# Kernel tuning notes

Measured on AMD Instinct MI355X. Metric: run time of the kernel, lower is better.

## Reference

```python
import jax, jax.numpy as jnp
import numpy as np

# Dimensions per init_kwargs / input_specs
B, N, C = 8192, 4, 2048          # tokens, expansion_rate, hidden_dim
SINKHORN_ITERS = 20
EPS = 1e-5
ALPHA_INIT = 0.01


def setup_inputs() -> dict:
    key = jax.random.key(0)
    k1, k2 = jax.random.split(key)
    return {
        "x_expanded": jax.random.normal(k1, (B, N, C), dtype=jnp.float32),
        "rmsnorm_weight": jnp.ones((C,), dtype=jnp.float32),   # init: ones
        "H_pre": jnp.zeros((N,), dtype=jnp.float32),            # init: zeros
        "H_post": jnp.zeros((N,), dtype=jnp.float32),           # init: zeros
        "H_res": ALPHA_INIT * jax.random.normal(k2, (N, N), dtype=jnp.float32),
    }


def _sinkhorn(M, iters, eps):
    """Iterative row/column normalization -> (approximately) doubly-stochastic."""
    def body(_, M):
        M = M / (jnp.sum(M, axis=1, keepdims=True) + eps)  # row normalize
        M = M / (jnp.sum(M, axis=0, keepdims=True) + eps)  # col normalize
        return M
    return jax.lax.fori_loop(0, iters, body, M)


def reference(x_expanded, rmsnorm_weight, H_pre, H_post, H_res):
    # RMSNorm over hidden dim C, per (token, branch)
    ms = jnp.mean(x_expanded * x_expanded, axis=-1, keepdims=True)  # [B, N, 1]
    x_norm = x_expanded * jax.lax.rsqrt(ms + EPS) * rmsnorm_weight  # [B, N, C]

    # Manifold-constrained residual mixing matrix (doubly stochastic via Sinkhorn)
    H = _sinkhorn(jnp.exp(H_res), SINKHORN_ITERS, EPS)              # [N, N]

    pre = jax.nn.sigmoid(H_pre)    # [N] input-aggregation weights
    post = jax.nn.sigmoid(H_post)  # [N] output-distribution weights

    # Aggregate normalized branches into a single stream, redistribute,
    # and add the Sinkhorn-mixed residual of the raw branches.
    x_agg = jnp.einsum('n,bnc->bc', pre, x_norm)                     # [B, C]
    y = jnp.einsum('mn,bnc->bmc', H, x_expanded) \
        + post[None, :, None] * x_agg[:, None, :]                    # [B, N, C]
    return y
```

## Files before the change

kernel.cpp:

```cpp
#include <hip/hip_runtime.h>
#include <math.h>

#define B_TOK 8192
#define NB 4
#define CH 2048
#define TPB 512
#define NBLK 1024
#define TOK_PER_BLK 8
#define SINK_ITERS 20
#define EPS 1e-5f

typedef float f32x4 __attribute__((ext_vector_type(4)));

__device__ __forceinline__ float bcast_first(float v) {
    return __uint_as_float(__builtin_amdgcn_readfirstlane(__float_as_uint(v)));
}
__device__ __forceinline__ float read_lane(float v, int l) {
    return __uint_as_float(__builtin_amdgcn_readlane(__float_as_uint(v), l));
}

__global__ __launch_bounds__(TPB) void mhc_fused(
    const float* __restrict__ x,
    const float* __restrict__ w,
    const float* __restrict__ H_pre,
    const float* __restrict__ H_post,
    const float* __restrict__ H_res,
    float* __restrict__ y)
{
    const int t = threadIdx.x;
    const int wave = t >> 6;
    const int lane = t & 63;
    const int b0 = blockIdx.x * TOK_PER_BLK;

    __shared__ f32x4 red4[2][TPB / 64];

    f32x4 xA0, xA1, xA2, xA3, xB0, xB1, xB2, xB3;
    auto xload = [&](int b, f32x4& d0, f32x4& d1, f32x4& d2, f32x4& d3) {
        const f32x4* p = (const f32x4*)x + (size_t)b * (NB * CH / 4) + t;
        d0 = __builtin_nontemporal_load(p);
        d1 = __builtin_nontemporal_load(p + (CH / 4));
        d2 = __builtin_nontemporal_load(p + 2 * (CH / 4));
        d3 = __builtin_nontemporal_load(p + 3 * (CH / 4));
    };
    xload(b0 + 0, xA0, xA1, xA2, xA3);
    xload(b0 + 1, xB0, xB1, xB2, xB3);
    const f32x4 wv = ((const f32x4*)w)[t];

    const int e = lane & 15;
    float v = expf(H_res[e]);
    #pragma unroll 1
    for (int it = 0; it < SINK_ITERS; ++it) {
        float s = v + __shfl_xor(v, 1);
        s += __shfl_xor(s, 2);
        v *= __builtin_amdgcn_rcpf(s + EPS);
        s = v + __shfl_xor(v, 4);
        s += __shfl_xor(s, 8);
        v *= __builtin_amdgcn_rcpf(s + EPS);
    }
    const float H00 = read_lane(v, 0),  H01 = read_lane(v, 1),
                H02 = read_lane(v, 2),  H03 = read_lane(v, 3);
    const float H10 = read_lane(v, 4),  H11 = read_lane(v, 5),
                H12 = read_lane(v, 6),  H13 = read_lane(v, 7);
    const float H20 = read_lane(v, 8),  H21 = read_lane(v, 9),
                H22 = read_lane(v, 10), H23 = read_lane(v, 11);
    const float H30 = read_lane(v, 12), H31 = read_lane(v, 13),
                H32 = read_lane(v, 14), H33 = read_lane(v, 15);

    const float pre0 = bcast_first(1.0f / (1.0f + expf(-H_pre[0])));
    const float pre1 = bcast_first(1.0f / (1.0f + expf(-H_pre[1])));
    const float pre2 = bcast_first(1.0f / (1.0f + expf(-H_pre[2])));
    const float pre3 = bcast_first(1.0f / (1.0f + expf(-H_pre[3])));
    const float ps0  = bcast_first(1.0f / (1.0f + expf(-H_post[0])));
    const float ps1  = bcast_first(1.0f / (1.0f + expf(-H_post[1])));
    const float ps2  = bcast_first(1.0f / (1.0f + expf(-H_post[2])));
    const float ps3  = bcast_first(1.0f / (1.0f + expf(-H_post[3])));

    auto process = [&](int b, f32x4 x0, f32x4 x1, f32x4 x2, f32x4 x3, int ph) {
        float s0 = x0.x * x0.x + x0.y * x0.y + x0.z * x0.z + x0.w * x0.w;
        float s1 = x1.x * x1.x + x1.y * x1.y + x1.z * x1.z + x1.w * x1.w;
        float s2 = x2.x * x2.x + x2.y * x2.y + x2.z * x2.z + x2.w * x2.w;
        float s3 = x3.x * x3.x + x3.y * x3.y + x3.z * x3.z + x3.w * x3.w;
        #pragma unroll
        for (int m = 1; m < 64; m <<= 1) {
            s0 += __shfl_xor(s0, m);
            s1 += __shfl_xor(s1, m);
            s2 += __shfl_xor(s2, m);
            s3 += __shfl_xor(s3, m);
        }
        if (lane == 0) {
            f32x4 pv = { s0, s1, s2, s3 };
            red4[ph][wave] = pv;
        }

        __builtin_amdgcn_sched_barrier(0);
        asm volatile("s_waitcnt lgkmcnt(0)" ::: "memory");
        __builtin_amdgcn_s_barrier();
        __builtin_amdgcn_sched_barrier(0);

        f32x4 r0 = red4[ph][0], r1 = red4[ph][1], r2 = red4[ph][2], r3 = red4[ph][3];
        f32x4 r4 = red4[ph][4], r5 = red4[ph][5], r6 = red4[ph][6], r7 = red4[ph][7];
        float t0 = ((r0.x + r1.x) + (r2.x + r3.x)) + ((r4.x + r5.x) + (r6.x + r7.x));
        float t1 = ((r0.y + r1.y) + (r2.y + r3.y)) + ((r4.y + r5.y) + (r6.y + r7.y));
        float t2 = ((r0.z + r1.z) + (r2.z + r3.z)) + ((r4.z + r5.z) + (r6.z + r7.z));
        float t3 = ((r0.w + r1.w) + (r2.w + r3.w)) + ((r4.w + r5.w) + (r6.w + r7.w));

        const float a0 = pre0 * rsqrtf(t0 * (1.0f / CH) + EPS);
        const float a1 = pre1 * rsqrtf(t1 * (1.0f / CH) + EPS);
        const float a2 = pre2 * rsqrtf(t2 * (1.0f / CH) + EPS);
        const float a3 = pre3 * rsqrtf(t3 * (1.0f / CH) + EPS);

        f32x4 wu;
        wu.x = wv.x * (a0 * x0.x + a1 * x1.x + a2 * x2.x + a3 * x3.x);
        wu.y = wv.y * (a0 * x0.y + a1 * x1.y + a2 * x2.y + a3 * x3.y);
        wu.z = wv.z * (a0 * x0.z + a1 * x1.z + a2 * x2.z + a3 * x3.z);
        wu.w = wv.w * (a0 * x0.w + a1 * x1.w + a2 * x2.w + a3 * x3.w);

        f32x4* yp = (f32x4*)y + (size_t)b * (NB * CH / 4) + t;
        f32x4 o;
        o.x = H00 * x0.x + H01 * x1.x + H02 * x2.x + H03 * x3.x + ps0 * wu.x;
        o.y = H00 * x0.y + H01 * x1.y + H02 * x2.y + H03 * x3.y + ps0 * wu.y;
        o.z = H00 * x0.z + H01 * x1.z + H02 * x2.z + H03 * x3.z + ps0 * wu.z;
        o.w = H00 * x0.w + H01 * x1.w + H02 * x2.w + H03 * x3.w + ps0 * wu.w;
        __builtin_nontemporal_store(o, yp);
        o.x = H10 * x0.x + H11 * x1.x + H12 * x2.x + H13 * x3.x + ps1 * wu.x;
        o.y = H10 * x0.y + H11 * x1.y + H12 * x2.y + H13 * x3.y + ps1 * wu.y;
        o.z = H10 * x0.z + H11 * x1.z + H12 * x2.z + H13 * x3.z + ps1 * wu.z;
        o.w = H10 * x0.w + H11 * x1.w + H12 * x2.w + H13 * x3.w + ps1 * wu.w;
        __builtin_nontemporal_store(o, yp + (CH / 4));
        o.x = H20 * x0.x + H21 * x1.x + H22 * x2.x + H23 * x3.x + ps2 * wu.x;
        o.y = H20 * x0.y + H21 * x1.y + H22 * x2.y + H23 * x3.y + ps2 * wu.y;
        o.z = H20 * x0.z + H21 * x1.z + H22 * x2.z + H23 * x3.z + ps2 * wu.z;
        o.w = H20 * x0.w + H21 * x1.w + H22 * x2.w + H23 * x3.w + ps2 * wu.w;
        __builtin_nontemporal_store(o, yp + 2 * (CH / 4));
        o.x = H30 * x0.x + H31 * x1.x + H32 * x2.x + H33 * x3.x + ps3 * wu.x;
        o.y = H30 * x0.y + H31 * x1.y + H32 * x2.y + H33 * x3.y + ps3 * wu.y;
        o.z = H30 * x0.z + H31 * x1.z + H32 * x2.z + H33 * x3.z + ps3 * wu.z;
        o.w = H30 * x0.w + H31 * x1.w + H32 * x2.w + H33 * x3.w + ps3 * wu.w;
        __builtin_nontemporal_store(o, yp + 3 * (CH / 4));
    };

    process(b0 + 0, xA0, xA1, xA2, xA3, 0);
    xload(b0 + 2, xA0, xA1, xA2, xA3);
    process(b0 + 1, xB0, xB1, xB2, xB3, 1);
    xload(b0 + 3, xB0, xB1, xB2, xB3);
    process(b0 + 2, xA0, xA1, xA2, xA3, 0);
    xload(b0 + 4, xA0, xA1, xA2, xA3);
    process(b0 + 3, xB0, xB1, xB2, xB3, 1);
    xload(b0 + 5, xB0, xB1, xB2, xB3);
    process(b0 + 4, xA0, xA1, xA2, xA3, 0);
    xload(b0 + 6, xA0, xA1, xA2, xA3);
    process(b0 + 5, xB0, xB1, xB2, xB3, 1);
    xload(b0 + 7, xB0, xB1, xB2, xB3);
    process(b0 + 6, xA0, xA1, xA2, xA3, 0);
    process(b0 + 7, xB0, xB1, xB2, xB3, 1);
}

extern "C" void kernel_launch(void* const* d_in, const int* in_sizes, int n_in,
                              void* d_out, int out_size, void* d_ws, size_t ws_size,
                              hipStream_t stream) {
    const float* x      = (const float*)d_in[0];
    const float* wgt    = (const float*)d_in[1];
    const float* h_pre  = (const float*)d_in[2];
    const float* h_post = (const float*)d_in[3];
    const float* h_res  = (const float*)d_in[4];
    float* y = (float*)d_out;

    mhc_fused<<<NBLK, TPB, 0, stream>>>(x, wgt, h_pre, h_post, h_res, y);
}
```

Measured before the change: 102.4 us.

## Assign one token per wave to remove block-level LDS reduction and barriers

```diff
diff --git a/kernel.cpp b/kernel.cpp
--- a/kernel.cpp
+++ b/kernel.cpp
@@ -1,12 +1,11 @@
 #include <hip/hip_runtime.h>
 #include <math.h>
 
-#define B_TOK 8192
 #define NB 4
 #define CH 2048
-#define TPB 512
-#define NBLK 1024
-#define TOK_PER_BLK 8
+#define TPB 256
+#define NBLK 512
+#define TOK_PER_WAVE 4
 #define SINK_ITERS 20
 #define EPS 1e-5f
 
@@ -19,7 +18,7 @@
     return __uint_as_float(__builtin_amdgcn_readlane(__float_as_uint(v), l));
 }
 
-__global__ __launch_bounds__(TPB) void mhc_fused(
+__global__ __launch_bounds__(TPB, 2) void mhc_wave(
     const float* __restrict__ x,
     const float* __restrict__ w,
     const float* __restrict__ H_pre,
@@ -30,21 +29,14 @@
     const int t = threadIdx.x;
     const int wave = t >> 6;
     const int lane = t & 63;
-    const int b0 = blockIdx.x * TOK_PER_BLK;
+    const int gw = blockIdx.x * (TPB / 64) + wave;
+    const int b0 = gw * TOK_PER_WAVE;
 
-    __shared__ f32x4 red4[2][TPB / 64];
-
-    f32x4 xA0, xA1, xA2, xA3, xB0, xB1, xB2, xB3;
-    auto xload = [&](int b, f32x4& d0, f32x4& d1, f32x4& d2, f32x4& d3) {
-        const f32x4* p = (const f32x4*)x + (size_t)b * (NB * CH / 4) + t;
-        d0 = __builtin_nontemporal_load(p);
-        d1 = __builtin_nontemporal_load(p + (CH / 4));
-        d2 = __builtin_nontemporal_load(p + 2 * (CH / 4));
-        d3 = __builtin_nontemporal_load(p + 3 * (CH / 4));
-    };
-    xload(b0 + 0, xA0, xA1, xA2, xA3);
-    xload(b0 + 1, xB0, xB1, xB2, xB3);
-    const f32x4 wv = ((const f32x4*)w)[t];
+    const f32x4* w4 = (const f32x4*)w;
+    f32x4 wv[8];
+    #pragma unroll
+    for (int k = 0; k < 8; ++k)
+        wv[k] = w4[lane + 64 * k];
 
     const int e = lane & 15;
     float v = expf(H_res[e]);
@@ -75,84 +67,68 @@
     const float ps2  = bcast_first(1.0f / (1.0f + expf(-H_post[2])));
     const float ps3  = bcast_first(1.0f / (1.0f + expf(-H_post[3])));
 
-    auto process = [&](int b, f32x4 x0, f32x4 x1, f32x4 x2, f32x4 x3, int ph) {
-        float s0 = x0.x * x0.x + x0.y * x0.y + x0.z * x0.z + x0.w * x0.w;
-        float s1 = x1.x * x1.x + x1.y * x1.y + x1.z * x1.z + x1.w * x1.w;
-        float s2 = x2.x * x2.x + x2.y * x2.y + x2.z * x2.z + x2.w * x2.w;
-        float s3 = x3.x * x3.x + x3.y * x3.y + x3.z * x3.z + x3.w * x3.w;
+    #pragma unroll 1
+    for (int tok = 0; tok < TOK_PER_WAVE; ++tok) {
+        const int b = b0 + tok;
+        const f32x4* xb = (const f32x4*)x + (size_t)b * (NB * CH / 4) + lane;
+
+        f32x4 xr[NB][8];
         #pragma unroll
-        for (int m = 1; m < 64; m <<= 1) {
-            s0 += __shfl_xor(s0, m);
-            s1 += __shfl_xor(s1, m);
-            s2 += __shfl_xor(s2, m);
-            s3 += __shfl_xor(s3, m);
-        }
-        if (lane == 0) {
-            f32x4 pv = { s0, s1, s2, s3 };
-            red4[ph][wave] = pv;
+        for (int n = 0; n < NB; ++n)
+            #pragma unroll
+            for (int k = 0; k < 8; ++k)
+                xr[n][k] = __builtin_nontemporal_load(xb + n * (CH / 4) + k * 64);
+
+        float ss[NB] = {0.f, 0.f, 0.f, 0.f};
+        #pragma unroll
+        for (int n = 0; n < NB; ++n) {
+            #pragma unroll
+            for (int k = 0; k < 8; ++k) {
+                f32x4 c = xr[n][k];
+                ss[n] += c.x * c.x + c.y * c.y + c.z * c.z + c.w * c.w;
+            }
         }
 
-        __builtin_amdgcn_sched_barrier(0);
-        asm volatile("s_waitcnt lgkmcnt(0)" ::: "memory");
-        __builtin_amdgcn_s_barrier();
-        __builtin_amdgcn_sched_barrier(0);
+        float x01 = (lane & 1) ? ss[1] : ss[0];
+        float y01 = (lane & 1) ? ss[0] : ss[1];
+        x01 += __shfl_xor(y01, 1);
+        float x23 = (lane & 1) ? ss[3] : ss[2];
+        float y23 = (lane & 1) ? ss[2] : ss[3];
+        x23 += __shfl_xor(y23, 1);
+        float z  = (lane & 2) ? x23 : x01;
+        float zz = (lane & 2) ? x01 : x23;
+        z += __shfl_xor(zz, 2);
+        z += __shfl_xor(z, 4);
+        z += __shfl_xor(z, 8);
+        z += __shfl_xor(z, 16);
+        z += __shfl_xor(z, 32);
 
-        f32x4 r0 = red4[ph][0], r1 = red4[ph][1], r2 = red4[ph][2], r3 = red4[ph][3];
-        f32x4 r4 = red4[ph][4], r5 = red4[ph][5], r6 = red4[ph][6], r7 = red4[ph][7];
-        float t0 = ((r0.x + r1.x) + (r2.x + r3.x)) + ((r4.x + r5.x) + (r6.x + r7.x));
-        float t1 = ((r0.y + r1.y) + (r2.y + r3.y)) + ((r4.y + r5.y) + (r6.y + r7.y));
-        float t2 = ((r0.z + r1.z) + (r2.z + r3.z)) + ((r4.z + r5.z) + (r6.z + r7.z));
-        float t3 = ((r0.w + r1.w) + (r2.w + r3.w)) + ((r4.w + r5.w) + (r6.w + r7.w));
+        const float t0 = read_lane(z, 0);
+        const float t1 = read_lane(z, 1);
+        const float t2 = read_lane(z, 2);
+        const float t3 = read_lane(z, 3);
 
         const float a0 = pre0 * rsqrtf(t0 * (1.0f / CH) + EPS);
         const float a1 = pre1 * rsqrtf(t1 * (1.0f / CH) + EPS);
         const float a2 = pre2 * rsqrtf(t2 * (1.0f / CH) + EPS);
         const float a3 = pre3 * rsqrtf(t3 * (1.0f / CH) + EPS);
 
-        f32x4 wu;
-        wu.x = wv.x * (a0 * x0.x + a1 * x1.x + a2 * x2.x + a3 * x3.x);
-        wu.y = wv.y * (a0 * x0.y + a1 * x1.y + a2 * x2.y + a3 * x3.y);
-        wu.z = wv.z * (a0 * x0.z + a1 * x1.z + a2 * x2.z + a3 * x3.z);
-        wu.w = wv.w * (a0 * x0.w + a1 * x1.w + a2 * x2.w + a3 * x3.w);
-
-        f32x4* yp = (f32x4*)y + (size_t)b * (NB * CH / 4) + t;
-        f32x4 o;
-        o.x = H00 * x0.x + H01 * x1.x + H02 * x2.x + H03 * x3.x + ps0 * wu.x;
-        o.y = H00 * x0.y + H01 * x1.y + H02 * x2.y + H03 * x3.y + ps0 * wu.y;
-        o.z = H00 * x0.z + H01 * x1.z + H02 * x2.z + H03 * x3.z + ps0 * wu.z;
-        o.w = H00 * x0.w + H01 * x1.w + H02 * x2.w + H03 * x3.w + ps0 * wu.w;
-        __builtin_nontemporal_store(o, yp);
-        o.x = H10 * x0.x + H11 * x1.x + H12 * x2.x + H13 * x3.x + ps1 * wu.x;
-        o.y = H10 * x0.y + H11 * x1.y + H12 * x2.y + H13 * x3.y + ps1 * wu.y;
-        o.z = H10 * x0.z + H11 * x1.z + H12 * x2.z + H13 * x3.z + ps1 * wu.z;
-        o.w = H10 * x0.w + H11 * x1.w + H12 * x2.w + H13 * x3.w + ps1 * wu.w;
-        __builtin_nontemporal_store(o, yp + (CH / 4));
-        o.x = H20 * x0.x + H21 * x1.x + H22 * x2.x + H23 * x3.x + ps2 * wu.x;
-        o.y = H20 * x0.y + H21 * x1.y + H22 * x2.y + H23 * x3.y + ps2 * wu.y;
-        o.z = H20 * x0.z + H21 * x1.z + H22 * x2.z + H23 * x3.z + ps2 * wu.z;
-        o.w = H20 * x0.w + H21 * x1.w + H22 * x2.w + H23 * x3.w + ps2 * wu.w;
-        __builtin_nontemporal_store(o, yp + 2 * (CH / 4));
-        o.x = H30 * x0.x + H31 * x1.x + H32 * x2.x + H33 * x3.x + ps3 * wu.x;
-        o.y = H30 * x0.y + H31 * x1.y + H32 * x2.y + H33 * x3.y + ps3 * wu.y;
-        o.z = H30 * x0.z + H31 * x1.z + H32 * x2.z + H33 * x3.z + ps3 * wu.z;
-        o.w = H30 * x0.w + H31 * x1.w + H32 * x2.w + H33 * x3.w + ps3 * wu.w;
-        __builtin_nontemporal_store(o, yp + 3 * (CH / 4));
-    };
-
-    process(b0 + 0, xA0, xA1, xA2, xA3, 0);
-    xload(b0 + 2, xA0, xA1, xA2, xA3);
-    process(b0 + 1, xB0, xB1, xB2, xB3, 1);
-    xload(b0 + 3, xB0, xB1, xB2, xB3);
-    process(b0 + 2, xA0, xA1, xA2, xA3, 0);
-    xload(b0 + 4, xA0, xA1, xA2, xA3);
-    process(b0 + 3, xB0, xB1, xB2, xB3, 1);
-    xload(b0 + 5, xB0, xB1, xB2, xB3);
-    process(b0 + 4, xA0, xA1, xA2, xA3, 0);
-    xload(b0 + 6, xA0, xA1, xA2, xA3);
-    process(b0 + 5, xB0, xB1, xB2, xB3, 1);
-    xload(b0 + 7, xB0, xB1, xB2, xB3);
-    process(b0 + 6, xA0, xA1, xA2, xA3, 0);
-    process(b0 + 7, xB0, xB1, xB2, xB3, 1);
+        f32x4* yb = (f32x4*)y + (size_t)b * (NB * CH / 4) + lane;
+        #pragma unroll
+        for (int k = 0; k < 8; ++k) {
+            const f32x4 c0 = xr[0][k], c1 = xr[1][k], c2 = xr[2][k], c3 = xr[3][k];
+            const f32x4 wu = wv[k] * (a0 * c0 + a1 * c1 + a2 * c2 + a3 * c3);
+            f32x4 o;
+            o = H00 * c0 + H01 * c1 + H02 * c2 + H03 * c3 + ps0 * wu;
+            __builtin_nontemporal_store(o, yb + 0 * (CH / 4) + k * 64);
+            o = H10 * c0 + H11 * c1 + H12 * c2 + H13 * c3 + ps1 * wu;
+            __builtin_nontemporal_store(o, yb + 1 * (CH / 4) + k * 64);
+            o = H20 * c0 + H21 * c1 + H22 * c2 + H23 * c3 + ps2 * wu;
+            __builtin_nontemporal_store(o, yb + 2 * (CH / 4) + k * 64);
+            o = H30 * c0 + H31 * c1 + H32 * c2 + H33 * c3 + ps3 * wu;
+            __builtin_nontemporal_store(o, yb + 3 * (CH / 4) + k * 64);
+        }
+    }
 }
 
 extern "C" void kernel_launch(void* const* d_in, const int* in_sizes, int n_in,
@@ -165,5 +141,5 @@
     const float* h_res  = (const float*)d_in[4];
     float* y = (float*)d_out;
 
-    mhc_fused<<<NBLK, TPB, 0, stream>>>(x, wgt, h_pre, h_post, h_res, y);
+    mhc_wave<<<NBLK, TPB, 0, stream>>>(x, wgt, h_pre, h_post, h_res, y);
 }
```

Result: slower. 113.9 us (+11.2%).
